# Performance work log

Hardware: AMD Instinct MI355X
Metric: run time of the kernel (lower is better)

The kernel has to match this reference:

```python
import jax, jax.numpy as jnp
import numpy as np

# Multi-scale AvgPool3d pyramid (stride 1, zero padding, count_include_pad=True as in torch)
KERNELS = [(1, 1, 1), (1, 5, 5), (3, 13, 13), (5, 23, 23), (7, 31, 31), (9, 41, 41)]
WEIGHTS = [w / 100.0 for w in [20, 20, 20, 20, 20, 20, 10, 10]]
EPS = 1e-7  # BatchDiceLoss epsilon


def avgpool3d(x, k):
    # x: [B, C, D, H, W]; separable sum-pool per axis then divide by full kernel size
    # (equivalent to torch AvgPool3d with count_include_pad=True, stride 1, pad=(k-1)//2)
    y = x
    for axis, ks in zip((2, 3, 4), k):
        if ks > 1:
            window = [1] * 5
            window[axis] = ks
            pad = [(0, 0)] * 5
            pad[axis] = (ks // 2, ks // 2)
            y = jax.lax.reduce_window(y, 0.0, jax.lax.add, tuple(window), (1,) * 5, tuple(pad))
    return y / float(np.prod(k))


def batch_dice(pred, target):
    # BatchDiceLoss([1.0]): single label channel 0, flattened over the whole batch
    p = pred[:, 0].reshape(-1)
    t = target[:, 0].reshape(-1)
    inter = jnp.sum(p * t)
    return 1.0 - (2.0 * inter) / (jnp.sum(p) + jnp.sum(t) + EPS)


def multi_scale_dc(pred, target):
    loss = 0.0
    for k in KERNELS:
        pp = avgpool3d(avgpool3d(pred, k), k)   # pool applied twice per scale
        tt = avgpool3d(avgpool3d(target, k), k)
        loss = loss + batch_dice(pp, tt)
    return loss / len(KERNELS)


def setup_inputs() -> dict:
    key = jax.random.key(0)
    ks = jax.random.split(key, 14)
    vol = (4, 1, 28, 160, 160)
    u = lambda k: jax.random.uniform(k, vol, dtype=jnp.float32)
    return {
        "pr_core_c": u(ks[0]),
        "pr_core_p": u(ks[1]),
        "gt_core": u(ks[2]),
        "pr_lesion_c": u(ks[3]),
        "pr_lesion_p": u(ks[4]),
        "gt_lesion": u(ks[5]),
        "pr_penu_c": u(ks[6]),
        "pr_penu_p": u(ks[7]),
        "gt_penu": u(ks[8]),
        "output": jax.random.uniform(ks[9], (4, 6, 28, 160, 160), dtype=jnp.float32),
        "off_core_c": jax.random.normal(ks[10], (4, 3), dtype=jnp.float32),
        "off_penu_p": jax.random.normal(ks[11], (4, 3), dtype=jnp.float32),
        "off_target_c": jax.random.normal(ks[12], (4, 3), dtype=jnp.float32),
        "off_target_p": jax.random.normal(ks[13], (4, 3), dtype=jnp.float32),
    }


def reference(pr_core_c, pr_core_p, gt_core, pr_lesion_c, pr_lesion_p, gt_lesion,
              pr_penu_c, pr_penu_p, gt_penu, output,
              off_core_c, off_penu_p, off_target_c, off_target_p):
    loss = WEIGHTS[0] * multi_scale_dc(pr_core_c, gt_core)
    loss += WEIGHTS[1] * multi_scale_dc(pr_core_p, gt_core)
    loss += WEIGHTS[2] * multi_scale_dc(pr_lesion_c, gt_lesion)
    loss += WEIGHTS[3] * multi_scale_dc(pr_lesion_p, gt_lesion)
    loss += WEIGHTS[4] * multi_scale_dc(pr_penu_c, gt_penu)
    loss += WEIGHTS[5] * multi_scale_dc(pr_penu_p, gt_penu)
    # temporal monotonicity penalty: mean(|diff| - diff) per consecutive time pair
    diff = output[:, 1:] - output[:, :-1]           # [B, T-1, D, H, W]
    loss += WEIGHTS[6] * jnp.sum(jnp.mean(jnp.abs(diff) - diff, axis=(0, 2, 3, 4)))
    loss += WEIGHTS[7] * jnp.mean(jnp.abs(off_core_c - off_target_c))
    loss += WEIGHTS[7] * jnp.mean(jnp.abs(off_penu_p - off_target_p))
    return loss
```

## Files before the change

kernel.cpp:

```cpp
#include <hip/hip_runtime.h>


#define DIMB 4
#define DIMD 28
#define DIMH 160
#define DIMW 160
#define HW   (DIMH * DIMW)
#define DHW  (DIMD * HW)
#define VOL_N (DIMB * DHW)
#define PGRID 640
#define NSLOTS 91
#define DICE_EPS 1e-7
#define TBL_OFF (480 * 1024)

__device__ __forceinline__ float u2f(int pos, int k, int L) {
    if (k == 1) return 1.f;
    int r = k >> 1;
    float s = 0.f;
    for (int j = max(pos - r, 0); j <= min(pos + r, L - 1); ++j)
        s += (float)(min(j + r, L - 1) - max(j - r, 0) + 1);
    return s / (float)(k * k);
}

__device__ __forceinline__ float wave_sum(float v) {
#pragma unroll
    for (int o = 1; o < 64; o <<= 1) v += __shfl_xor(v, o, 64);
    return v;
}

template<int K>
__device__ __forceinline__ void box4_col(float (&x)[28]) {
    constexpr int R = K / 2;
    constexpr float INVK = 1.f / (float)K;
#pragma unroll
    for (int p = 0; p < 4; ++p) {
        float y[28];
        float s = 0.f;
#pragma unroll
        for (int j = 0; j <= R; ++j) s += x[j];
        y[0] = s;
#pragma unroll
        for (int i = 1; i < 28; ++i) {
            if (i + R < 28) s += x[i + R];
            if (i - R - 1 >= 0) s -= x[i - R - 1];
            y[i] = s;
        }
#pragma unroll
        for (int i = 0; i < 28; ++i) x[i] = y[i] * INVK;
    }
}

template<int K>
__device__ __forceinline__ void hstore(const float (&raw)[40],
                                       unsigned char* __restrict__ ob,
                                       int l, int c, int wl, int h0)
{
    constexpr int R = K / 2;
    constexpr float INVK = 1.f / (float)K;
    float ox[40];
#pragma unroll
    for (int i = 0; i < 40; ++i) ox[i] = raw[i];
#pragma unroll
    for (int pass = 0; pass < 4; ++pass) {
        float lo[R], hi[R];
#pragma unroll
        for (int i = 0; i < R; ++i) {
            float a = __shfl(ox[40 - R + i], l - 16, 64);
            lo[i] = (c == 0) ? 0.f : a;
            float b = __shfl(ox[i], l + 16, 64);
            hi[i] = (c == 3) ? 0.f : b;
        }
#define HWIN(j) ((j) < R ? lo[(j)] : ((j) < R + 40 ? ox[(j) - R] : hi[(j) - R - 40]))
        float out[40];
        float s = 0.f;
#pragma unroll
        for (int j = 0; j <= 2 * R; ++j) s += HWIN(j);
        out[0] = s * INVK;
#pragma unroll
        for (int i = 1; i < 40; ++i) {
            s += HWIN(i + 2 * R) - HWIN(i - 1);
            out[i] = s * INVK;
        }
#undef HWIN
#pragma unroll
        for (int i = 0; i < 40; ++i) ox[i] = out[i];
    }
#pragma unroll
    for (int i = 0; i < 40; ++i)
        ob[(h0 + i) * DIMW + wl] = (unsigned char)__float2uint_rn(ox[i] * 255.f);
}

__global__ __launch_bounds__(256) void hpool_mono(const float* __restrict__ g0,
    const float* __restrict__ g1, const float* __restrict__ g2,
    const float* __restrict__ o6, unsigned char* __restrict__ bufs,
    double* __restrict__ partials, float* __restrict__ tbl)
{
    __shared__ float redSm[4];
    int bx = blockIdx.x;
    if (bx < 840) {
        int u = bx * 2 + (threadIdx.x >> 7);
        int tt = threadIdx.x & 127;
        int g = u / 560, r = u - g * 560;
        int bd = r / 5, wt = r - bd * 5;
        const float* in = (g == 0) ? g0 : (g == 1) ? g1 : g2;
        int l = tt & 63, v = tt >> 6;
        int c = l >> 4, wl = v * 16 + (l & 15), h0 = c * 40;
        const float* base = in + (size_t)bd * HW + wt * 32;
        float raw[40];
#pragma unroll
        for (int i = 0; i < 40; ++i) raw[i] = base[(h0 + i) * DIMW + wl];
        unsigned char* ob = bufs + (size_t)g * 5 * VOL_N + (size_t)bd * HW + wt * 32;
        hstore<5> (raw, ob + 0 * (size_t)VOL_N, l, c, wl, h0);
        hstore<13>(raw, ob + 1 * (size_t)VOL_N, l, c, wl, h0);
        hstore<23>(raw, ob + 2 * (size_t)VOL_N, l, c, wl, h0);
        hstore<31>(raw, ob + 3 * (size_t)VOL_N, l, c, wl, h0);
        hstore<41>(raw, ob + 4 * (size_t)VOL_N, l, c, wl, h0);
    } else if (bx < 1480) {
        int mb = bx - 840;
        const int N4 = VOL_N / 4, PB = N4 / DIMB;
        float acc = 0.f;
        const float4* p = (const float4*)o6;
        for (int i = mb * 256 + threadIdx.x; i < N4; i += PGRID * 256) {
            int b = i / PB, r4 = i - b * PB;
            size_t a = (size_t)(b * 6) * PB + r4;
            float4 prev = p[a];
#pragma unroll
            for (int cc = 1; cc < 6; ++cc) {
                float4 cur = p[a + (size_t)cc * PB];
                acc += fmaxf(prev.x - cur.x, 0.f) + fmaxf(prev.y - cur.y, 0.f)
                     + fmaxf(prev.z - cur.z, 0.f) + fmaxf(prev.w - cur.w, 0.f);
                prev = cur;
            }
        }
        float rv = wave_sum(acc * 2.f);
        int lane = threadIdx.x & 63, wid = threadIdx.x >> 6;
        if (lane == 0) redSm[wid] = rv;
        __syncthreads();
        if (threadIdx.x == 0)
            partials[(size_t)90 * PGRID + mb] =
                (double)redSm[0] + redSm[1] + redSm[2] + redSm[3];
    } else {
        const int KDa[6] = {1, 1, 3, 5, 7, 9};
        const int KHa[6] = {1, 5, 13, 23, 31, 41};
        for (int e = threadIdx.x; e < 1128; e += 256) {
            if (e < 960) tbl[e] = u2f(e % 160, KHa[e / 160], DIMH);
            else {
                int q = e - 960;
                tbl[e] = u2f(q % 28, KDa[q / 28], DIMD);
            }
        }
    }
}

template<int K>
__device__ __forceinline__ void wpool_to_S(const unsigned char* __restrict__ tb,
    float (*S)[164], int t, int l, int rr, int c, bool act)
{
    constexpr int R = K / 2;
    float ox[20];
#pragma unroll
    for (int i = 0; i < 20; ++i) ox[i] = 0.f;
    if (act) {
        unsigned int u[5];
#pragma unroll
        for (int q = 0; q < 5; ++q) u[q] = *(const unsigned int*)(tb + 4 * q);
#pragma unroll
        for (int q = 0; q < 5; ++q) {
#pragma unroll
            for (int j = 0; j < 4; ++j)
                ox[4 * q + j] = (float)((u[q] >> (8 * j)) & 0xFFu);
        }
    }
#pragma unroll
    for (int pass = 0; pass < 4; ++pass) {
        const float scl = (pass == 0) ? (1.f / ((float)K * 255.f)) : (1.f / (float)K);
        float lo[R], hi[R];
#pragma unroll
        for (int i = 0; i < R; ++i) {
            float a = __shfl(ox[20 - R + i], l - 1, 64);
            lo[i] = (c == 0) ? 0.f : a;
            float b = __shfl(ox[i], l + 1, 64);
            hi[i] = (c == 7) ? 0.f : b;
        }
#define WWIN(j) ((j) < R ? lo[(j)] : ((j) < R + 20 ? ox[(j) - R] : hi[(j) - R - 20]))
        float out[20];
        float s = 0.f;
#pragma unroll
        for (int j = 0; j <= 2 * R; ++j) s += WWIN(j);
        out[0] = s * scl;
#pragma unroll
        for (int i = 1; i < 20; ++i) {
            s += WWIN(i + 2 * R) - WWIN(i - 1);
            out[i] = s * scl;
        }
#undef WWIN
#pragma unroll
        for (int i = 0; i < 20; ++i) ox[i] = out[i];
    }
    if (act) {
#pragma unroll
        for (int i = 0; i < 20; ++i) S[rr][c * 20 + i] = ox[i];
    }
    __syncthreads();
}

template<int K, int KD>
__device__ __forceinline__ void wd_scale(const unsigned char* __restrict__ tb,
    const float4* __restrict__ c4, const float4* __restrict__ p4, int base4,
    float (*S)[164], float* red2, int t, int l, int wid, int rr, int c, bool act,
    double* __restrict__ partials, int slot_c, int slot_p, int bh)
{
    wpool_to_S<K>(tb, S, t, l, rr, c, act);
    if constexpr (KD > 1) {
        if (t < DIMW) {
            float col[28];
#pragma unroll
            for (int j = 0; j < 28; ++j) col[j] = S[j][t];
            box4_col<KD>(col);
#pragma unroll
            for (int j = 0; j < 28; ++j) S[j][t] = col[j];
        }
        __syncthreads();
    }
    float aic = 0.f, aip = 0.f;
    for (int e4 = t; e4 < 1120; e4 += 256) {
        int dd = e4 / 40, w4 = e4 - dd * 40;
        int fi = base4 + dd * (HW / 4) + w4;
        float4 vc = c4[fi], vp = p4[fi];
        const float4 sv = *(const float4*)&S[dd][4 * w4];
        aic += vc.x * sv.x + vc.y * sv.y + vc.z * sv.z + vc.w * sv.w;
        aip += vp.x * sv.x + vp.y * sv.y + vp.z * sv.z + vp.w * sv.w;
    }
    float r1 = wave_sum(aic), r2 = wave_sum(aip);
    if (l == 0) { red2[wid * 2] = r1; red2[wid * 2 + 1] = r2; }
    __syncthreads();
    if (t < 2) {
        double rv = (double)red2[t] + red2[2 + t] + red2[4 + t] + red2[6 + t];
        partials[(size_t)(t == 0 ? slot_c : slot_p) * PGRID + bh] = rv;
    }
}

__global__ __launch_bounds__(256) void wd_dot0(const unsigned char* __restrict__ bufs,
    const float* __restrict__ pc0, const float* __restrict__ pp0,
    const float* __restrict__ pc1, const float* __restrict__ pp1,
    const float* __restrict__ pc2, const float* __restrict__ pp2,
    const float* __restrict__ tr0, const float* __restrict__ tr1,
    const float* __restrict__ tr2, const float* __restrict__ tbl,
    double* __restrict__ partials)
{
    __shared__ __align__(16) float S[DIMD][164];
    __shared__ float redS[4][24];
    int bx = blockIdx.x;
    int t = threadIdx.x;
    int q = bx / 1920, r = bx - q * 1920;
    int g = r / PGRID, bh = r - g * PGRID;
    int b = bh / DIMH, h = bh - b * DIMH;
    const float* pc = (g == 0) ? pc0 : (g == 1) ? pc1 : pc2;
    const float* pp = (g == 0) ? pp0 : (g == 1) ? pp1 : pp2;
    size_t base0 = (size_t)b * DHW + (size_t)h * DIMW;
    int base4 = b * (DHW / 4) + h * 40;
    const float4* c4 = (const float4*)pc;
    const float4* p4 = (const float4*)pp;
    int l = t & 63, wid = t >> 6;
    int rr = wid * 7 + (l >> 3), c = l & 7;
    bool act = (l < 56);
    int sbuf = (q < 4) ? (4 - q) : 0;
    const unsigned char* tb = bufs + (size_t)(g * 5 + sbuf) * VOL_N
                            + base0 + (size_t)rr * HW + c * 20;

    if (q < 4) {
        int s = 5 - q;
        int slot_c = (2 * g) * 6 + s, slot_p = (2 * g + 1) * 6 + s;
        switch (q) {
            case 0: wd_scale<41, 9>(tb, c4, p4, base4, S, &redS[0][0], t, l, wid, rr, c, act, partials, slot_c, slot_p, bh); break;
            case 1: wd_scale<31, 7>(tb, c4, p4, base4, S, &redS[0][0], t, l, wid, rr, c, act, partials, slot_c, slot_p, bh); break;
            case 2: wd_scale<23, 5>(tb, c4, p4, base4, S, &redS[0][0], t, l, wid, rr, c, act, partials, slot_c, slot_p, bh); break;
            default: wd_scale<13, 3>(tb, c4, p4, base4, S, &redS[0][0], t, l, wid, rr, c, act, partials, slot_c, slot_p, bh); break;
        }
        return;
    }

    const float* tr = (g == 0) ? tr0 : (g == 1) ? tr1 : tr2;
    const float4* t4 = (const float4*)tr;
    wpool_to_S<5>(tb, S, t, l, rr, c, act);
    float vals[22];
#pragma unroll
    for (int i = 0; i < 22; ++i) vals[i] = 0.f;
    for (int e4 = t; e4 < 1120; e4 += 256) {
        int dd = e4 / 40, w4 = e4 - dd * 40;
        int fi = base4 + dd * (HW / 4) + w4;
        float4 vc = c4[fi], vp = p4[fi], vt = t4[fi];
        const float4 sv = *(const float4*)&S[dd][4 * w4];
        vals[0] += vc.x*sv.x + vc.y*sv.y + vc.z*sv.z + vc.w*sv.w;
        vals[1] += vp.x*sv.x + vp.y*sv.y + vp.z*sv.z + vp.w*sv.w;
        vals[2] += vc.x*vt.x + vc.y*vt.y + vc.z*vt.z + vc.w*vt.w;
        vals[3] += vp.x*vt.x + vp.y*vt.y + vp.z*vt.z + vp.w*vt.w;
#pragma unroll
        for (int s = 0; s < 6; ++s) {
            float cdh = tbl[960 + s * 28 + dd];
            const float4 cw = *(const float4*)(tbl + s * 160 + 4 * w4);
            vals[4 + s]  += cdh * (cw.x*vc.x + cw.y*vc.y + cw.z*vc.z + cw.w*vc.w);
            vals[10 + s] += cdh * (cw.x*vp.x + cw.y*vp.y + cw.z*vp.z + cw.w*vp.w);
            vals[16 + s] += cdh * (cw.x*vt.x + cw.y*vt.y + cw.z*vt.z + cw.w*vt.w);
        }
    }
#pragma unroll
    for (int i = 0; i < 22; ++i) {
        float rv = wave_sum(vals[i]);
        if (l == 0) redS[wid][i] = rv;
    }
    __syncthreads();
    if (t < 22) {
        double rv = (double)redS[0][t] + redS[1][t] + redS[2][t] + redS[3][t];
        double fac = 1.0;
        int slot;
        if (t == 0) slot = (2 * g) * 6 + 1;
        else if (t == 1) slot = (2 * g + 1) * 6 + 1;
        else if (t == 2) slot = (2 * g) * 6;
        else if (t == 3) slot = (2 * g + 1) * 6;
        else {
            int i = t - 4, vv = i / 6, s = i % 6;
            fac = (double)tbl[s * 160 + h];
            slot = (vv == 0) ? 36 + (2 * g) * 6 + s
                 : (vv == 1) ? 36 + (2 * g + 1) * 6 + s
                             : 72 + g * 6 + s;
        }
        partials[(size_t)slot * PGRID + bh] = rv * fac;
    }
}

__global__ __launch_bounds__(64) void fin_pre(const double* __restrict__ partials,
                                              double* __restrict__ ssum)
{
    int slot = blockIdx.x, t = threadIdx.x;
    double a = 0.0;
    for (int i = t; i < PGRID; i += 64) a += partials[(size_t)slot * PGRID + i];
#pragma unroll
    for (int o = 1; o < 64; o <<= 1) a += __shfl_xor(a, o, 64);
    if (t == 0) ssum[slot] = a;
}

__global__ void finalize(const double* __restrict__ ssum,
                         const float* __restrict__ off_a,
                         const float* __restrict__ off_b,
                         const float* __restrict__ off_ta,
                         const float* __restrict__ off_tb,
                         float* __restrict__ out)
{
    if (threadIdx.x == 0) {
        double loss = 0.0;
        for (int pair = 0; pair < 6; ++pair) {
            for (int s = 0; s < 6; ++s) {
                double inter = ssum[pair * 6 + s];
                double sp = ssum[36 + pair * 6 + s];
                double st = ssum[72 + (pair / 2) * 6 + s];
                loss += 0.2 * (1.0 - 2.0 * inter / (sp + st + DICE_EPS)) / 6.0;
            }
        }
        loss += 0.1 * (ssum[90] / (double)VOL_N);
        double oa = 0.0, ob = 0.0;
        for (int i = 0; i < 12; ++i) {
            oa += fabs((double)off_a[i] - (double)off_ta[i]);
            ob += fabs((double)off_b[i] - (double)off_tb[i]);
        }
        loss += 0.1 * (oa / 12.0) + 0.1 * (ob / 12.0);
        out[0] = (float)loss;
    }
}

extern "C" void kernel_launch(void* const* d_in, const int* in_sizes, int n_in,
                              void* d_out, int out_size, void* d_ws, size_t ws_size,
                              hipStream_t stream)
{
    double* partials = (double*)d_ws;
    double* ssum = partials + (size_t)NSLOTS * PGRID;
    float* tbl = (float*)((char*)d_ws + TBL_OFF);
    unsigned char* bufs = (unsigned char*)d_ws + 512 * 1024;

    const float* pred[6] = {(const float*)d_in[0], (const float*)d_in[1],
                            (const float*)d_in[3], (const float*)d_in[4],
                            (const float*)d_in[6], (const float*)d_in[7]};
    const float* gt[3] = {(const float*)d_in[2], (const float*)d_in[5],
                          (const float*)d_in[8]};

    hpool_mono<<<1481, 256, 0, stream>>>(gt[0], gt[1], gt[2],
                                         (const float*)d_in[9], bufs, partials, tbl);
    wd_dot0<<<9600, 256, 0, stream>>>(bufs, pred[0], pred[1], pred[2], pred[3],
                                      pred[4], pred[5], gt[0], gt[1], gt[2],
                                      tbl, partials);
    fin_pre<<<NSLOTS, 64, 0, stream>>>(partials, ssum);
    finalize<<<1, 64, 0, stream>>>(ssum,
                                   (const float*)d_in[10], (const float*)d_in[11],
                                   (const float*)d_in[12], (const float*)d_in[13],
                                   (float*)d_out);
}
```

Baseline: 135.6 us.

## Move monotonicity reduction to dot kernel, prefetch pred loads, remap block order

Moves the temporal monotonicity reduction out of the horizontal pooling kernel and into the first 640 blocks of the dot kernel, so the pooling kernel only does pooling and table setup. The dot kernel now issues the u8 pooled-buffer loads and the pred float4 loads into registers before the width-pooling shuffles, so memory latency overlaps with pooling arithmetic. Block indices are also permuted so neighbouring blocks handle different scales and slices, which spreads the heavy and light scales across the GPU. The cost is higher register pressure from holding ten float4 values per thread, which may lower occupancy.

```diff
diff --git a/kernel.cpp b/kernel.cpp
--- a/kernel.cpp
+++ b/kernel.cpp
@@ -90,12 +90,10 @@
         ob[(h0 + i) * DIMW + wl] = (unsigned char)__float2uint_rn(ox[i] * 255.f);
 }
 
-__global__ __launch_bounds__(256) void hpool_mono(const float* __restrict__ g0,
+__global__ __launch_bounds__(256) void hpool_tbl(const float* __restrict__ g0,
     const float* __restrict__ g1, const float* __restrict__ g2,
-    const float* __restrict__ o6, unsigned char* __restrict__ bufs,
-    double* __restrict__ partials, float* __restrict__ tbl)
-{
-    __shared__ float redSm[4];
+    unsigned char* __restrict__ bufs, float* __restrict__ tbl)
+{
     int bx = blockIdx.x;
     if (bx < 840) {
         int u = bx * 2 + (threadIdx.x >> 7);
@@ -115,30 +113,6 @@
         hstore<23>(raw, ob + 2 * (size_t)VOL_N, l, c, wl, h0);
         hstore<31>(raw, ob + 3 * (size_t)VOL_N, l, c, wl, h0);
         hstore<41>(raw, ob + 4 * (size_t)VOL_N, l, c, wl, h0);
-    } else if (bx < 1480) {
-        int mb = bx - 840;
-        const int N4 = VOL_N / 4, PB = N4 / DIMB;
-        float acc = 0.f;
-        const float4* p = (const float4*)o6;
-        for (int i = mb * 256 + threadIdx.x; i < N4; i += PGRID * 256) {
-            int b = i / PB, r4 = i - b * PB;
-            size_t a = (size_t)(b * 6) * PB + r4;
-            float4 prev = p[a];
-#pragma unroll
-            for (int cc = 1; cc < 6; ++cc) {
-                float4 cur = p[a + (size_t)cc * PB];
-                acc += fmaxf(prev.x - cur.x, 0.f) + fmaxf(prev.y - cur.y, 0.f)
-                     + fmaxf(prev.z - cur.z, 0.f) + fmaxf(prev.w - cur.w, 0.f);
-                prev = cur;
-            }
-        }
-        float rv = wave_sum(acc * 2.f);
-        int lane = threadIdx.x & 63, wid = threadIdx.x >> 6;
-        if (lane == 0) redSm[wid] = rv;
-        __syncthreads();
-        if (threadIdx.x == 0)
-            partials[(size_t)90 * PGRID + mb] =
-                (double)redSm[0] + redSm[1] + redSm[2] + redSm[3];
     } else {
         const int KDa[6] = {1, 1, 3, 5, 7, 9};
         const int KHa[6] = {1, 5, 13, 23, 31, 41};
@@ -153,23 +127,16 @@
 }
 
 template<int K>
-__device__ __forceinline__ void wpool_to_S(const unsigned char* __restrict__ tb,
-    float (*S)[164], int t, int l, int rr, int c, bool act)
+__device__ __forceinline__ void wpool_S(const unsigned int (&ub)[5],
+    float (*S)[164], int l, int rr, int c, bool act)
 {
     constexpr int R = K / 2;
     float ox[20];
 #pragma unroll
-    for (int i = 0; i < 20; ++i) ox[i] = 0.f;
-    if (act) {
-        unsigned int u[5];
-#pragma unroll
-        for (int q = 0; q < 5; ++q) u[q] = *(const unsigned int*)(tb + 4 * q);
-#pragma unroll
-        for (int q = 0; q < 5; ++q) {
-#pragma unroll
-            for (int j = 0; j < 4; ++j)
-                ox[4 * q + j] = (float)((u[q] >> (8 * j)) & 0xFFu);
-        }
+    for (int q = 0; q < 5; ++q) {
+#pragma unroll
+        for (int j = 0; j < 4; ++j)
+            ox[4 * q + j] = (float)((ub[q] >> (8 * j)) & 0xFFu);
     }
 #pragma unroll
     for (int pass = 0; pass < 4; ++pass) {
@@ -205,12 +172,12 @@
 }
 
 template<int K, int KD>
-__device__ __forceinline__ void wd_scale(const unsigned char* __restrict__ tb,
-    const float4* __restrict__ c4, const float4* __restrict__ p4, int base4,
+__device__ __forceinline__ void wd_scale(const unsigned int (&ub)[5],
+    const float4 (&rc)[5], const float4 (&rp)[5],
     float (*S)[164], float* red2, int t, int l, int wid, int rr, int c, bool act,
     double* __restrict__ partials, int slot_c, int slot_p, int bh)
 {
-    wpool_to_S<K>(tb, S, t, l, rr, c, act);
+    wpool_S<K>(ub, S, l, rr, c, act);
     if constexpr (KD > 1) {
         if (t < DIMW) {
             float col[28];
@@ -223,13 +190,13 @@
         __syncthreads();
     }
     float aic = 0.f, aip = 0.f;
-    for (int e4 = t; e4 < 1120; e4 += 256) {
-        int dd = e4 / 40, w4 = e4 - dd * 40;
-        int fi = base4 + dd * (HW / 4) + w4;
-        float4 vc = c4[fi], vp = p4[fi];
+#pragma unroll
+    for (int qq = 0; qq < 5; ++qq) {
+        int e4c = min(t + 256 * qq, 1119);
+        int dd = e4c / 40, w4 = e4c - dd * 40;
         const float4 sv = *(const float4*)&S[dd][4 * w4];
-        aic += vc.x * sv.x + vc.y * sv.y + vc.z * sv.z + vc.w * sv.w;
-        aip += vp.x * sv.x + vp.y * sv.y + vp.z * sv.z + vp.w * sv.w;
+        aic += rc[qq].x * sv.x + rc[qq].y * sv.y + rc[qq].z * sv.z + rc[qq].w * sv.w;
+        aip += rp[qq].x * sv.x + rp[qq].y * sv.y + rp[qq].z * sv.z + rp[qq].w * sv.w;
     }
     float r1 = wave_sum(aic), r2 = wave_sum(aip);
     if (l == 0) { red2[wid * 2] = r1; red2[wid * 2 + 1] = r2; }
@@ -245,15 +212,45 @@
     const float* __restrict__ pc1, const float* __restrict__ pp1,
     const float* __restrict__ pc2, const float* __restrict__ pp2,
     const float* __restrict__ tr0, const float* __restrict__ tr1,
-    const float* __restrict__ tr2, const float* __restrict__ tbl,
-    double* __restrict__ partials)
+    const float* __restrict__ tr2, const float* __restrict__ o6,
+    const float* __restrict__ tbl, double* __restrict__ partials)
 {
     __shared__ __align__(16) float S[DIMD][164];
     __shared__ float redS[4][24];
-    int bx = blockIdx.x;
+    int bx0 = blockIdx.x;
     int t = threadIdx.x;
-    int q = bx / 1920, r = bx - q * 1920;
-    int g = r / PGRID, bh = r - g * PGRID;
+
+    if (bx0 < 640) {
+        int mb = bx0;
+        const int N4 = VOL_N / 4, PB = N4 / DIMB;
+        float acc = 0.f;
+        const float4* p = (const float4*)o6;
+        for (int i = mb * 256 + t; i < N4; i += PGRID * 256) {
+            int b = i / PB, r4 = i - b * PB;
+            size_t a = (size_t)(b * 6) * PB + r4;
+            float4 prev = p[a];
+#pragma unroll
+            for (int cc = 1; cc < 6; ++cc) {
+                float4 cur = p[a + (size_t)cc * PB];
+                acc += fmaxf(prev.x - cur.x, 0.f) + fmaxf(prev.y - cur.y, 0.f)
+                     + fmaxf(prev.z - cur.z, 0.f) + fmaxf(prev.w - cur.w, 0.f);
+                prev = cur;
+            }
+        }
+        float rv = wave_sum(acc * 2.f);
+        int lane = t & 63, wid = t >> 6;
+        if (lane == 0) redS[wid][0] = rv;
+        __syncthreads();
+        if (t == 0)
+            partials[(size_t)90 * PGRID + mb] =
+                (double)redS[0][0] + redS[1][0] + redS[2][0] + redS[3][0];
+        return;
+    }
+
+    int bxx = bx0 - 640;
+    int w = (bxx & 7) * 1200 + (bxx >> 3);
+    int u = w / 5, q = w - u * 5;
+    int g = u / PGRID, bh = u - g * PGRID;
     int b = bh / DIMH, h = bh - b * DIMH;
     const float* pc = (g == 0) ? pc0 : (g == 1) ? pc1 : pc2;
     const float* pp = (g == 0) ? pp0 : (g == 1) ? pp1 : pp2;
@@ -268,39 +265,61 @@
     const unsigned char* tb = bufs + (size_t)(g * 5 + sbuf) * VOL_N
                             + base0 + (size_t)rr * HW + c * 20;
 
+    unsigned int ub[5] = {0u, 0u, 0u, 0u, 0u};
+    if (act) {
+#pragma unroll
+        for (int qq = 0; qq < 5; ++qq) ub[qq] = *(const unsigned int*)(tb + 4 * qq);
+    }
+    const float4 Z4 = make_float4(0.f, 0.f, 0.f, 0.f);
+    float4 rc[5], rp[5];
+#pragma unroll
+    for (int qq = 0; qq < 5; ++qq) {
+        int e4 = t + 256 * qq;
+        bool v = e4 < 1120;
+        int e4c = min(e4, 1119);
+        int dd = e4c / 40, w4 = e4c - dd * 40;
+        int fi = base4 + dd * (HW / 4) + w4;
+        rc[qq] = v ? c4[fi] : Z4;
+        rp[qq] = v ? p4[fi] : Z4;
+    }
+
     if (q < 4) {
         int s = 5 - q;
         int slot_c = (2 * g) * 6 + s, slot_p = (2 * g + 1) * 6 + s;
         switch (q) {
-            case 0: wd_scale<41, 9>(tb, c4, p4, base4, S, &redS[0][0], t, l, wid, rr, c, act, partials, slot_c, slot_p, bh); break;
-            case 1: wd_scale<31, 7>(tb, c4, p4, base4, S, &redS[0][0], t, l, wid, rr, c, act, partials, slot_c, slot_p, bh); break;
-            case 2: wd_scale<23, 5>(tb, c4, p4, base4, S, &redS[0][0], t, l, wid, rr, c, act, partials, slot_c, slot_p, bh); break;
-            default: wd_scale<13, 3>(tb, c4, p4, base4, S, &redS[0][0], t, l, wid, rr, c, act, partials, slot_c, slot_p, bh); break;
+            case 0: wd_scale<41, 9>(ub, rc, rp, S, &redS[0][0], t, l, wid, rr, c, act, partials, slot_c, slot_p, bh); break;
+            case 1: wd_scale<31, 7>(ub, rc, rp, S, &redS[0][0], t, l, wid, rr, c, act, partials, slot_c, slot_p, bh); break;
+            case 2: wd_scale<23, 5>(ub, rc, rp, S, &redS[0][0], t, l, wid, rr, c, act, partials, slot_c, slot_p, bh); break;
+            default: wd_scale<13, 3>(ub, rc, rp, S, &redS[0][0], t, l, wid, rr, c, act, partials, slot_c, slot_p, bh); break;
         }
         return;
     }
 
     const float* tr = (g == 0) ? tr0 : (g == 1) ? tr1 : tr2;
     const float4* t4 = (const float4*)tr;
-    wpool_to_S<5>(tb, S, t, l, rr, c, act);
+    wpool_S<5>(ub, S, l, rr, c, act);
     float vals[22];
 #pragma unroll
     for (int i = 0; i < 22; ++i) vals[i] = 0.f;
-    for (int e4 = t; e4 < 1120; e4 += 256) {
-        int dd = e4 / 40, w4 = e4 - dd * 40;
+#pragma unroll
+    for (int qq = 0; qq < 5; ++qq) {
+        int e4 = t + 256 * qq;
+        bool v = e4 < 1120;
+        int e4c = min(e4, 1119);
+        int dd = e4c / 40, w4 = e4c - dd * 40;
         int fi = base4 + dd * (HW / 4) + w4;
-        float4 vc = c4[fi], vp = p4[fi], vt = t4[fi];
+        float4 vt = v ? t4[fi] : Z4;
         const float4 sv = *(const float4*)&S[dd][4 * w4];
-        vals[0] += vc.x*sv.x + vc.y*sv.y + vc.z*sv.z + vc.w*sv.w;
-        vals[1] += vp.x*sv.x + vp.y*sv.y + vp.z*sv.z + vp.w*sv.w;
-        vals[2] += vc.x*vt.x + vc.y*vt.y + vc.z*vt.z + vc.w*vt.w;
-        vals[3] += vp.x*vt.x + vp.y*vt.y + vp.z*vt.z + vp.w*vt.w;
+        vals[0] += rc[qq].x*sv.x + rc[qq].y*sv.y + rc[qq].z*sv.z + rc[qq].w*sv.w;
+        vals[1] += rp[qq].x*sv.x + rp[qq].y*sv.y + rp[qq].z*sv.z + rp[qq].w*sv.w;
+        vals[2] += rc[qq].x*vt.x + rc[qq].y*vt.y + rc[qq].z*vt.z + rc[qq].w*vt.w;
+        vals[3] += rp[qq].x*vt.x + rp[qq].y*vt.y + rp[qq].z*vt.z + rp[qq].w*vt.w;
 #pragma unroll
         for (int s = 0; s < 6; ++s) {
             float cdh = tbl[960 + s * 28 + dd];
             const float4 cw = *(const float4*)(tbl + s * 160 + 4 * w4);
-            vals[4 + s]  += cdh * (cw.x*vc.x + cw.y*vc.y + cw.z*vc.z + cw.w*vc.w);
-            vals[10 + s] += cdh * (cw.x*vp.x + cw.y*vp.y + cw.z*vp.z + cw.w*vp.w);
+            vals[4 + s]  += cdh * (cw.x*rc[qq].x + cw.y*rc[qq].y + cw.z*rc[qq].z + cw.w*rc[qq].w);
+            vals[10 + s] += cdh * (cw.x*rp[qq].x + cw.y*rp[qq].y + cw.z*rp[qq].z + cw.w*rp[qq].w);
             vals[16 + s] += cdh * (cw.x*vt.x + cw.y*vt.y + cw.z*vt.z + cw.w*vt.w);
         }
     }
@@ -383,11 +402,10 @@
     const float* gt[3] = {(const float*)d_in[2], (const float*)d_in[5],
                           (const float*)d_in[8]};
 
-    hpool_mono<<<1481, 256, 0, stream>>>(gt[0], gt[1], gt[2],
-                                         (const float*)d_in[9], bufs, partials, tbl);
-    wd_dot0<<<9600, 256, 0, stream>>>(bufs, pred[0], pred[1], pred[2], pred[3],
-                                      pred[4], pred[5], gt[0], gt[1], gt[2],
-                                      tbl, partials);
+    hpool_tbl<<<841, 256, 0, stream>>>(gt[0], gt[1], gt[2], bufs, tbl);
+    wd_dot0<<<10240, 256, 0, stream>>>(bufs, pred[0], pred[1], pred[2], pred[3],
+                                       pred[4], pred[5], gt[0], gt[1], gt[2],
+                                       (const float*)d_in[9], tbl, partials);
     fin_pre<<<NSLOTS, 64, 0, stream>>>(partials, ssum);
     finalize<<<1, 64, 0, stream>>>(ssum,
                                    (const float*)d_in[10], (const float*)d_in[11],
```

Measured after the change: 310.4 us. +129.0%, slower.

## Move monotonicity reduction into second kernel and remap block-to-work order

Applied to the files above, without the earlier changes.

The temporal-monotonicity reduction over the 6-channel output moves out of the first (horizontal pool) kernel and into the front 640 blocks of the main pooling/dot kernel, so the first kernel only does pooling and table building. The main kernel's block index is also remapped so consecutive blocks interleave the five scale cases (q) and spread across groups, which changes scheduling and cache locality. The per-pass scaling in the width pool is folded into a single multiply at the store. Together these aim to shorten the critical first kernel and balance work across CUs, at the cost of slightly different float rounding and a longer second kernel.

```diff
diff --git a/kernel.cpp b/kernel.cpp
--- a/kernel.cpp
+++ b/kernel.cpp
@@ -90,12 +90,10 @@
         ob[(h0 + i) * DIMW + wl] = (unsigned char)__float2uint_rn(ox[i] * 255.f);
 }
 
-__global__ __launch_bounds__(256) void hpool_mono(const float* __restrict__ g0,
+__global__ __launch_bounds__(256) void hpool_tbl(const float* __restrict__ g0,
     const float* __restrict__ g1, const float* __restrict__ g2,
-    const float* __restrict__ o6, unsigned char* __restrict__ bufs,
-    double* __restrict__ partials, float* __restrict__ tbl)
-{
-    __shared__ float redSm[4];
+    unsigned char* __restrict__ bufs, float* __restrict__ tbl)
+{
     int bx = blockIdx.x;
     if (bx < 840) {
         int u = bx * 2 + (threadIdx.x >> 7);
@@ -115,30 +113,6 @@
         hstore<23>(raw, ob + 2 * (size_t)VOL_N, l, c, wl, h0);
         hstore<31>(raw, ob + 3 * (size_t)VOL_N, l, c, wl, h0);
         hstore<41>(raw, ob + 4 * (size_t)VOL_N, l, c, wl, h0);
-    } else if (bx < 1480) {
-        int mb = bx - 840;
-        const int N4 = VOL_N / 4, PB = N4 / DIMB;
-        float acc = 0.f;
-        const float4* p = (const float4*)o6;
-        for (int i = mb * 256 + threadIdx.x; i < N4; i += PGRID * 256) {
-            int b = i / PB, r4 = i - b * PB;
-            size_t a = (size_t)(b * 6) * PB + r4;
-            float4 prev = p[a];
-#pragma unroll
-            for (int cc = 1; cc < 6; ++cc) {
-                float4 cur = p[a + (size_t)cc * PB];
-                acc += fmaxf(prev.x - cur.x, 0.f) + fmaxf(prev.y - cur.y, 0.f)
-                     + fmaxf(prev.z - cur.z, 0.f) + fmaxf(prev.w - cur.w, 0.f);
-                prev = cur;
-            }
-        }
-        float rv = wave_sum(acc * 2.f);
-        int lane = threadIdx.x & 63, wid = threadIdx.x >> 6;
-        if (lane == 0) redSm[wid] = rv;
-        __syncthreads();
-        if (threadIdx.x == 0)
-            partials[(size_t)90 * PGRID + mb] =
-                (double)redSm[0] + redSm[1] + redSm[2] + redSm[3];
     } else {
         const int KDa[6] = {1, 1, 3, 5, 7, 9};
         const int KHa[6] = {1, 5, 13, 23, 31, 41};
@@ -157,6 +131,7 @@
     float (*S)[164], int t, int l, int rr, int c, bool act)
 {
     constexpr int R = K / 2;
+    const float INV = 1.0f / (255.0f * (float)K * (float)K * (float)K * (float)K);
     float ox[20];
 #pragma unroll
     for (int i = 0; i < 20; ++i) ox[i] = 0.f;
@@ -173,7 +148,6 @@
     }
 #pragma unroll
     for (int pass = 0; pass < 4; ++pass) {
-        const float scl = (pass == 0) ? (1.f / ((float)K * 255.f)) : (1.f / (float)K);
         float lo[R], hi[R];
 #pragma unroll
         for (int i = 0; i < R; ++i) {
@@ -187,11 +161,11 @@
         float s = 0.f;
 #pragma unroll
         for (int j = 0; j <= 2 * R; ++j) s += WWIN(j);
-        out[0] = s * scl;
+        out[0] = s;
 #pragma unroll
         for (int i = 1; i < 20; ++i) {
             s += WWIN(i + 2 * R) - WWIN(i - 1);
-            out[i] = s * scl;
+            out[i] = s;
         }
 #undef WWIN
 #pragma unroll
@@ -199,7 +173,7 @@
     }
     if (act) {
 #pragma unroll
-        for (int i = 0; i < 20; ++i) S[rr][c * 20 + i] = ox[i];
+        for (int i = 0; i < 20; ++i) S[rr][c * 20 + i] = ox[i] * INV;
     }
     __syncthreads();
 }
@@ -245,15 +219,45 @@
     const float* __restrict__ pc1, const float* __restrict__ pp1,
     const float* __restrict__ pc2, const float* __restrict__ pp2,
     const float* __restrict__ tr0, const float* __restrict__ tr1,
-    const float* __restrict__ tr2, const float* __restrict__ tbl,
-    double* __restrict__ partials)
+    const float* __restrict__ tr2, const float* __restrict__ o6,
+    const float* __restrict__ tbl, double* __restrict__ partials)
 {
     __shared__ __align__(16) float S[DIMD][164];
     __shared__ float redS[4][24];
-    int bx = blockIdx.x;
+    int bx0 = blockIdx.x;
     int t = threadIdx.x;
-    int q = bx / 1920, r = bx - q * 1920;
-    int g = r / PGRID, bh = r - g * PGRID;
+
+    if (bx0 < 640) {
+        int mb = bx0;
+        const int N4 = VOL_N / 4, PB = N4 / DIMB;
+        float acc = 0.f;
+        const float4* p = (const float4*)o6;
+        for (int i = mb * 256 + t; i < N4; i += PGRID * 256) {
+            int b = i / PB, r4 = i - b * PB;
+            size_t a = (size_t)(b * 6) * PB + r4;
+            float4 prev = p[a];
+#pragma unroll
+            for (int cc = 1; cc < 6; ++cc) {
+                float4 cur = p[a + (size_t)cc * PB];
+                acc += fmaxf(prev.x - cur.x, 0.f) + fmaxf(prev.y - cur.y, 0.f)
+                     + fmaxf(prev.z - cur.z, 0.f) + fmaxf(prev.w - cur.w, 0.f);
+                prev = cur;
+            }
+        }
+        float rv = wave_sum(acc * 2.f);
+        int lane = t & 63, wid = t >> 6;
+        if (lane == 0) redS[wid][0] = rv;
+        __syncthreads();
+        if (t == 0)
+            partials[(size_t)90 * PGRID + mb] =
+                (double)redS[0][0] + redS[1][0] + redS[2][0] + redS[3][0];
+        return;
+    }
+
+    int bxx = bx0 - 640;
+    int w = (bxx & 7) * 1200 + (bxx >> 3);
+    int u = w / 5, q = w - u * 5;
+    int g = u / PGRID, bh = u - g * PGRID;
     int b = bh / DIMH, h = bh - b * DIMH;
     const float* pc = (g == 0) ? pc0 : (g == 1) ? pc1 : pc2;
     const float* pp = (g == 0) ? pp0 : (g == 1) ? pp1 : pp2;
@@ -383,11 +387,10 @@
     const float* gt[3] = {(const float*)d_in[2], (const float*)d_in[5],
                           (const float*)d_in[8]};
 
-    hpool_mono<<<1481, 256, 0, stream>>>(gt[0], gt[1], gt[2],
-                                         (const float*)d_in[9], bufs, partials, tbl);
-    wd_dot0<<<9600, 256, 0, stream>>>(bufs, pred[0], pred[1], pred[2], pred[3],
-                                      pred[4], pred[5], gt[0], gt[1], gt[2],
-                                      tbl, partials);
+    hpool_tbl<<<841, 256, 0, stream>>>(gt[0], gt[1], gt[2], bufs, tbl);
+    wd_dot0<<<10240, 256, 0, stream>>>(bufs, pred[0], pred[1], pred[2], pred[3],
+                                       pred[4], pred[5], gt[0], gt[1], gt[2],
+                                       (const float*)d_in[9], tbl, partials);
     fin_pre<<<NSLOTS, 64, 0, stream>>>(partials, ssum);
     finalize<<<1, 64, 0, stream>>>(ssum,
                                    (const float*)d_in[10], (const float*)d_in[11],
```

Measured after the change: 135.7 us. No clear change (+0.1%).
